# Performance work log

Measured on AMD Instinct MI355X. Metric: run time of the kernel, lower is better.

The kernel has to match this reference:

```python
import jax, jax.numpy as jnp
import numpy as np

WINDOW = 128
LOOK_BACKWARD = 1
LOOK_FORWARD = 0  # causal=True -> look_forward defaults to 0
THETA = 10000.0


def look_around(x, backward=LOOK_BACKWARD, forward=LOOK_FORWARD, pad_value=-1):
    # x: (b, w, n, ...). Pad along window axis, concat shifted slices along token axis.
    w = x.shape[1]
    pad_width = [(0, 0)] * x.ndim
    pad_width[1] = (backward, forward)
    padded = jnp.pad(x, pad_width, constant_values=pad_value)
    return jnp.concatenate([padded[:, i:i + w] for i in range(forward + backward + 1)], axis=2)


def rotate_half(x):
    x1, x2 = jnp.split(x, 2, axis=-1)
    return jnp.concatenate((-x2, x1), axis=-1)


def setup_inputs() -> dict:
    key = jax.random.key(0)
    kq, kk, kv = jax.random.split(key, 3)
    shape = (32, 4096, 64)
    return {
        "q": jax.random.normal(kq, shape, dtype=jnp.float32),
        "k": jax.random.normal(kk, shape, dtype=jnp.float32),
        "v": jax.random.normal(kv, shape, dtype=jnp.float32),
    }


def reference(q, k, v):
    b, n, d = q.shape
    scale = d ** -0.5
    w = n // WINDOW

    bq = q.reshape(b, w, WINDOW, d) * scale
    bk = look_around(k.reshape(b, w, WINDOW, d), pad_value=-1.0)
    bv = look_around(v.reshape(b, w, WINDOW, d), pad_value=-1.0)
    j = bk.shape[2]  # (1 + look_backward + look_forward) * WINDOW = 256

    # rotary pos emb (SinusoidalEmbeddings, no xpos -> scale = 1)
    inv_freq = 1.0 / (THETA ** (jnp.arange(0, d, 2, dtype=jnp.float32) / d))
    t = jnp.arange(j, dtype=jnp.float32)
    freqs = jnp.einsum('i,j->ij', t, inv_freq)
    freqs = jnp.concatenate((freqs, freqs), axis=-1)  # (j, d)
    q_freqs = freqs[-WINDOW:]  # queries align to the last WINDOW positions
    bq = bq * jnp.cos(q_freqs) + rotate_half(bq) * jnp.sin(q_freqs)
    bk = bk * jnp.cos(freqs) + rotate_half(bk) * jnp.sin(freqs)

    # position bookkeeping for masks
    seq = jnp.arange(n)
    b_t = seq.reshape(1, w, WINDOW)           # (1, w, i)
    bq_t = b_t[..., :, None]                  # (1, w, i, 1)
    bq_k = look_around(b_t, pad_value=-1)[..., None, :]  # (1, w, 1, j)
    pad_mask = bq_k == -1
    causal_mask = bq_t < bq_k

    sim = jnp.einsum('bwie,bwje->bwij', bq, bk)  # (b, w, i, j)
    mask_value = -jnp.finfo(sim.dtype).max
    sim = jnp.where(causal_mask | pad_mask, mask_value, sim)

    attn = jax.nn.softmax(sim, axis=-1)
    out = jnp.einsum('bwij,bwje->bwie', attn, bv)
    return out.reshape(b, n, d)
```

## Files before the change

kernel.cpp:

```cpp
#include <hip/hip_runtime.h>
#include <hip/hip_bf16.h>

#define BDIM 512

typedef __attribute__((ext_vector_type(8))) _Float16 f16x8;
typedef __attribute__((ext_vector_type(4))) _Float16 f16x4;
typedef __attribute__((ext_vector_type(4))) float f32x4;

__global__ __launch_bounds__(512, 4)
void la_kernel(const float* __restrict__ qg, const float* __restrict__ kg,
               const float* __restrict__ vg, float* __restrict__ outg)
{
    __shared__ _Float16 Ks[2][128][72];
    __shared__ _Float16 Vt[2][64][140];

    const int wp = blockIdx.x, bb = blockIdx.y;
    const int tid = threadIdx.x;
    const int wv = tid >> 6, lane = tid & 63, g = lane >> 4, c = lane & 15;
    const int base = 256 * wp - 128;
    const float NEG = -3.0e38f;
    const float NLT32 = -0.28782313662425572f;

    const int cbK = (tid & 7) << 2;
    float invfK[4];
    #pragma unroll
    for (int u = 0; u < 4; ++u) invfK[u] = __expf((float)(cbK + u) * NLT32);
    float invfQ[8];
    #pragma unroll
    for (int u = 0; u < 8; ++u) invfQ[u] = __expf((float)(8 * g + u) * NLT32);

    const int jqV = tid >> 4, eqV = tid & 15;
    const int colbV = ((jqV & 24) << 2) + 8 * (jqV & 3) + 4 * ((jqV >> 2) & 1);

    auto stage = [&](int mm) {
        int sl = mm & 1;
        #pragma unroll
        for (int it = 0; it < 2; ++it) {
            int j = (tid + it * 512) >> 3;
            int t = 128 * mm + j;
            const float* p = kg + ((size_t)bb * 4096 + base + t) * 64 + cbK;
            float4 x1 = *(const float4*)p;
            float4 x2 = *(const float4*)(p + 32);
            const float* x1p = &x1.x;
            const float* x2p = &x2.x;
            f16x4 lo, hi;
            #pragma unroll
            for (int u = 0; u < 4; ++u) {
                float sn, cs; __sincosf((float)t * invfK[u], &sn, &cs);
                lo[u] = (_Float16)(x1p[u] * cs - x2p[u] * sn);
                hi[u] = (_Float16)(x2p[u] * cs + x1p[u] * sn);
            }
            *(f16x4*)&Ks[sl][j][cbK]      = lo;
            *(f16x4*)&Ks[sl][j][cbK + 32] = hi;
        }
        float4 x[4];
        #pragma unroll
        for (int w = 0; w < 4; ++w)
            x[w] = *(const float4*)(vg + ((size_t)bb * 4096 + base + 128 * mm + 4 * jqV + w) * 64 + 4 * eqV);
        #pragma unroll
        for (int u = 0; u < 4; ++u) {
            f16x4 o;
            o[0] = (_Float16)((const float*)&x[0])[u];
            o[1] = (_Float16)((const float*)&x[1])[u];
            o[2] = (_Float16)((const float*)&x[2])[u];
            o[3] = (_Float16)((const float*)&x[3])[u];
            *(f16x4*)&Vt[sl][4 * eqV + u][colbV] = o;
        }
    };

    auto computeWin = [&](int wi) {
        const int qrow = tid < 0 ? 0 : (wv * 16 + c);
        const int tq = 128 * (wi + 1) + qrow;

        f16x8 qa0, qa1;
        {
            const float* p = qg + ((size_t)bb * 4096 + base + tq) * 64 + 8 * g;
            float4 a0 = *(const float4*)p;
            float4 a1 = *(const float4*)(p + 4);
            float4 b0 = *(const float4*)(p + 32);
            float4 b1 = *(const float4*)(p + 36);
            float ra[8] = {a0.x,a0.y,a0.z,a0.w,a1.x,a1.y,a1.z,a1.w};
            float rb[8] = {b0.x,b0.y,b0.z,b0.w,b1.x,b1.y,b1.z,b1.w};
            #pragma unroll
            for (int u = 0; u < 8; ++u) {
                float sn, cs; __sincosf((float)tq * invfQ[u], &sn, &cs);
                float a = ra[u] * 0.125f, b = rb[u] * 0.125f;
                qa0[u] = (_Float16)(a * cs - b * sn);
                qa1[u] = (_Float16)(b * cs + a * sn);
            }
        }

        f32x4 accO[4];
        #pragma unroll
        for (int nt = 0; nt < 4; ++nt) accO[nt] = (f32x4){0.f,0.f,0.f,0.f};
        float m = NEG, s = 0.f;

        #pragma unroll 1
        for (int mm = wi; mm <= wi + 1; ++mm) {
            if (wp == 0 && mm == 0) continue;
            const int sl = mm & 1;
            const bool causal = (mm == wi + 1);

            #pragma unroll
            for (int ch = 0; ch < 2; ++ch) {
                f32x4 acc[4];
                #pragma unroll
                for (int jt = 0; jt < 4; ++jt) acc[jt] = (f32x4){0.f,0.f,0.f,0.f};

                #pragma unroll
                for (int jt = 0; jt < 4; ++jt) {
                    int row = ch * 64 + jt * 16 + c;
                    f16x8 kb0 = *(const f16x8*)&Ks[sl][row][8 * g];
                    f16x8 kb1 = *(const f16x8*)&Ks[sl][row][32 + 8 * g];
                    acc[jt] = __builtin_amdgcn_mfma_f32_16x16x32_f16(kb0, qa0, acc[jt], 0, 0, 0);
                    acc[jt] = __builtin_amdgcn_mfma_f32_16x16x32_f16(kb1, qa1, acc[jt], 0, 0, 0);
                }

                if (causal) {
                    #pragma unroll
                    for (int jt = 0; jt < 4; ++jt)
                        #pragma unroll
                        for (int r = 0; r < 4; ++r) {
                            int jj = ch * 64 + jt * 16 + 4 * g + r;
                            if (jj > qrow) acc[jt][r] = NEG;
                        }
                }

                float mx = NEG;
                #pragma unroll
                for (int jt = 0; jt < 4; ++jt)
                    #pragma unroll
                    for (int r = 0; r < 4; ++r) mx = fmaxf(mx, acc[jt][r]);
                mx = fmaxf(mx, __shfl_xor(mx, 16));
                mx = fmaxf(mx, __shfl_xor(mx, 32));

                float mnew = fmaxf(m, mx);
                float alpha = __expf(m - mnew);

                float ps = 0.f;
                f16x8 pa[2];
                #pragma unroll
                for (int jt = 0; jt < 4; ++jt)
                    #pragma unroll
                    for (int r = 0; r < 4; ++r) {
                        float p = __expf(acc[jt][r] - mnew);
                        ps += p;
                        pa[jt >> 1][(jt & 1) * 4 + r] = (_Float16)p;
                    }
                ps += __shfl_xor(ps, 16);
                ps += __shfl_xor(ps, 32);

                s = s * alpha + ps;
                m = mnew;

                float alphaD[4];
                #pragma unroll
                for (int r = 0; r < 4; ++r)
                    alphaD[r] = __shfl(alpha, (lane & 48) | (4 * g + r));
                #pragma unroll
                for (int nt = 0; nt < 4; ++nt)
                    #pragma unroll
                    for (int r = 0; r < 4; ++r) accO[nt][r] *= alphaD[r];

                #pragma unroll
                for (int st = 0; st < 2; ++st) {
                    #pragma unroll
                    for (int nt = 0; nt < 4; ++nt) {
                        f16x8 vb = *(const f16x8*)&Vt[sl][nt * 16 + c][ch * 64 + st * 32 + 8 * g];
                        accO[nt] = __builtin_amdgcn_mfma_f32_16x16x32_f16(pa[st], vb, accO[nt], 0, 0, 0);
                    }
                }
            }
        }

        float rcp = 1.0f / s;
        float rcpD[4];
        #pragma unroll
        for (int r = 0; r < 4; ++r)
            rcpD[r] = __shfl(rcp, (lane & 48) | (4 * g + r));

        float* op = outg + ((size_t)bb * 4096 + base + 128 * (wi + 1) + wv * 16) * 64;
        #pragma unroll
        for (int nt = 0; nt < 4; ++nt)
            #pragma unroll
            for (int r = 0; r < 4; ++r)
                op[(size_t)(4 * g + r) * 64 + nt * 16 + c] = accO[nt][r] * rcpD[r];
    };

    if (wp > 0) stage(0);
    stage(1);
    __syncthreads();
    computeWin(0);
    __syncthreads();
    stage(2);
    __syncthreads();
    computeWin(1);
}

extern "C" void kernel_launch(void* const* d_in, const int* in_sizes, int n_in,
                              void* d_out, int out_size, void* d_ws, size_t ws_size,
                              hipStream_t stream) {
    (void)in_sizes; (void)n_in; (void)out_size; (void)d_ws; (void)ws_size;
    const float* q = (const float*)d_in[0];
    const float* k = (const float*)d_in[1];
    const float* v = (const float*)d_in[2];
    float* out = (float*)d_out;
    dim3 grid(16, 32);
    la_kernel<<<grid, BDIM, 0, stream>>>(q, k, v, out);
}
```

Before: 34.00 us.

## Prefetch third K/V chunk into registers during first window compute

The K and V global loads for the third chunk are now issued before the first window's compute, held in registers, and rotated and written to shared memory only after that compute finishes. The Q load for window 0 is hoisted before the barrier, and the Q load for window 1 is moved ahead of the final barrier. This is meant to hide global-memory latency behind the MFMA work instead of stalling between the two window computations. It adds about 32 registers per thread of live prefetch data, which could limit occupancy under launch_bounds(512,4).

```diff
diff --git a/kernel.cpp b/kernel.cpp
--- a/kernel.cpp
+++ b/kernel.cpp
@@ -20,6 +20,7 @@
     const int base = 256 * wp - 128;
     const float NEG = -3.0e38f;
     const float NLT32 = -0.28782313662425572f;
+    const size_t rowb = (size_t)bb * 4096;
 
     const int cbK = (tid & 7) << 2;
     float invfK[4];
@@ -32,13 +33,15 @@
     const int jqV = tid >> 4, eqV = tid & 15;
     const int colbV = ((jqV & 24) << 2) + 8 * (jqV & 3) + 4 * ((jqV >> 2) & 1);
 
+    const int qrow = wv * 16 + c;
+
     auto stage = [&](int mm) {
         int sl = mm & 1;
         #pragma unroll
         for (int it = 0; it < 2; ++it) {
             int j = (tid + it * 512) >> 3;
             int t = 128 * mm + j;
-            const float* p = kg + ((size_t)bb * 4096 + base + t) * 64 + cbK;
+            const float* p = kg + (rowb + base + t) * 64 + cbK;
             float4 x1 = *(const float4*)p;
             float4 x2 = *(const float4*)(p + 32);
             const float* x1p = &x1.x;
@@ -56,7 +59,7 @@
         float4 x[4];
         #pragma unroll
         for (int w = 0; w < 4; ++w)
-            x[w] = *(const float4*)(vg + ((size_t)bb * 4096 + base + 128 * mm + 4 * jqV + w) * 64 + 4 * eqV);
+            x[w] = *(const float4*)(vg + (rowb + base + 128 * mm + 4 * jqV + w) * 64 + 4 * eqV);
         #pragma unroll
         for (int u = 0; u < 4; ++u) {
             f16x4 o;
@@ -68,28 +71,25 @@
         }
     };
 
-    auto computeWin = [&](int wi) {
-        const int qrow = tid < 0 ? 0 : (wv * 16 + c);
+    auto loadQ = [&](int wi, f16x8& qa0, f16x8& qa1) {
         const int tq = 128 * (wi + 1) + qrow;
-
-        f16x8 qa0, qa1;
-        {
-            const float* p = qg + ((size_t)bb * 4096 + base + tq) * 64 + 8 * g;
-            float4 a0 = *(const float4*)p;
-            float4 a1 = *(const float4*)(p + 4);
-            float4 b0 = *(const float4*)(p + 32);
-            float4 b1 = *(const float4*)(p + 36);
-            float ra[8] = {a0.x,a0.y,a0.z,a0.w,a1.x,a1.y,a1.z,a1.w};
-            float rb[8] = {b0.x,b0.y,b0.z,b0.w,b1.x,b1.y,b1.z,b1.w};
-            #pragma unroll
-            for (int u = 0; u < 8; ++u) {
-                float sn, cs; __sincosf((float)tq * invfQ[u], &sn, &cs);
-                float a = ra[u] * 0.125f, b = rb[u] * 0.125f;
-                qa0[u] = (_Float16)(a * cs - b * sn);
-                qa1[u] = (_Float16)(b * cs + a * sn);
-            }
-        }
-
+        const float* p = qg + (rowb + base + tq) * 64 + 8 * g;
+        float4 a0 = *(const float4*)p;
+        float4 a1 = *(const float4*)(p + 4);
+        float4 b0 = *(const float4*)(p + 32);
+        float4 b1 = *(const float4*)(p + 36);
+        float ra[8] = {a0.x,a0.y,a0.z,a0.w,a1.x,a1.y,a1.z,a1.w};
+        float rb[8] = {b0.x,b0.y,b0.z,b0.w,b1.x,b1.y,b1.z,b1.w};
+        #pragma unroll
+        for (int u = 0; u < 8; ++u) {
+            float sn, cs; __sincosf((float)tq * invfQ[u], &sn, &cs);
+            float a = ra[u] * 0.125f, b = rb[u] * 0.125f;
+            qa0[u] = (_Float16)(a * cs - b * sn);
+            qa1[u] = (_Float16)(b * cs + a * sn);
+        }
+    };
+
+    auto computeWin = [&](int wi, f16x8 qa0, f16x8 qa1) {
         f32x4 accO[4];
         #pragma unroll
         for (int nt = 0; nt < 4; ++nt) accO[nt] = (f32x4){0.f,0.f,0.f,0.f};
@@ -179,7 +179,7 @@
         for (int r = 0; r < 4; ++r)
             rcpD[r] = __shfl(rcp, (lane & 48) | (4 * g + r));
 
-        float* op = outg + ((size_t)bb * 4096 + base + 128 * (wi + 1) + wv * 16) * 64;
+        float* op = outg + (rowb + base + 128 * (wi + 1) + wv * 16) * 64;
         #pragma unroll
         for (int nt = 0; nt < 4; ++nt)
             #pragma unroll
@@ -189,12 +189,60 @@
 
     if (wp > 0) stage(0);
     stage(1);
+
+    f16x8 qA, qB;
+    loadQ(0, qA, qB);
+
+    float4 kx[4], vx[4];
+    {
+        #pragma unroll
+        for (int it = 0; it < 2; ++it) {
+            int j = (tid + it * 512) >> 3;
+            const float* p = kg + (rowb + base + 256 + j) * 64 + cbK;
+            kx[2 * it]     = *(const float4*)p;
+            kx[2 * it + 1] = *(const float4*)(p + 32);
+        }
+        #pragma unroll
+        for (int w = 0; w < 4; ++w)
+            vx[w] = *(const float4*)(vg + (rowb + base + 256 + 4 * jqV + w) * 64 + 4 * eqV);
+    }
+
     __syncthreads();
-    computeWin(0);
+    computeWin(0, qA, qB);
     __syncthreads();
-    stage(2);
+
+    {
+        #pragma unroll
+        for (int it = 0; it < 2; ++it) {
+            int j = (tid + it * 512) >> 3;
+            int t = 256 + j;
+            const float* x1p = (const float*)&kx[2 * it];
+            const float* x2p = (const float*)&kx[2 * it + 1];
+            f16x4 lo, hi;
+            #pragma unroll
+            for (int u = 0; u < 4; ++u) {
+                float sn, cs; __sincosf((float)t * invfK[u], &sn, &cs);
+                lo[u] = (_Float16)(x1p[u] * cs - x2p[u] * sn);
+                hi[u] = (_Float16)(x2p[u] * cs + x1p[u] * sn);
+            }
+            *(f16x4*)&Ks[0][j][cbK]      = lo;
+            *(f16x4*)&Ks[0][j][cbK + 32] = hi;
+        }
+        #pragma unroll
+        for (int u = 0; u < 4; ++u) {
+            f16x4 o;
+            o[0] = (_Float16)((const float*)&vx[0])[u];
+            o[1] = (_Float16)((const float*)&vx[1])[u];
+            o[2] = (_Float16)((const float*)&vx[2])[u];
+            o[3] = (_Float16)((const float*)&vx[3])[u];
+            *(f16x4*)&Vt[0][4 * eqV + u][colbV] = o;
+        }
+    }
+
+    loadQ(1, qA, qB);
+
     __syncthreads();
-    computeWin(1);
+    computeWin(1, qA, qB);
 }
 
 extern "C" void kernel_launch(void* const* d_in, const int* in_sizes, int n_in,
```

Measured after the change: 36.38 us. 1.07x slower.

## Skip fully masked causal chunks, use exp2 softmax, prefetch Q earlier

Applied to the files above, without the earlier changes.

Waves whose query rows all sit below the second 64-key chunk of the diagonal window now skip that chunk's QK and PV MFMAs entirely. The softmax switches to exp2 by folding log2(e) into the Q scale. It also skips the rescale of the output accumulator when no row's running max grows, tested wave-wide with __all. Q loads are issued before K/V staging and the barriers so global latency overlaps other work. The cost is extra branching plus slightly different rounding from the base-2 exponent path.

```diff
diff --git a/kernel.cpp b/kernel.cpp
--- a/kernel.cpp
+++ b/kernel.cpp
@@ -6,6 +6,8 @@
 typedef __attribute__((ext_vector_type(8))) _Float16 f16x8;
 typedef __attribute__((ext_vector_type(4))) _Float16 f16x4;
 typedef __attribute__((ext_vector_type(4))) float f32x4;
+
+#define EXP2F(x) __builtin_amdgcn_exp2f(x)
 
 __global__ __launch_bounds__(512, 4)
 void la_kernel(const float* __restrict__ qg, const float* __restrict__ kg,
@@ -20,6 +22,8 @@
     const int base = 256 * wp - 128;
     const float NEG = -3.0e38f;
     const float NLT32 = -0.28782313662425572f;
+    const float QSCALE = 0.125f * 1.4426950408889634f;
+    const size_t rowb = (size_t)bb * 4096;
 
     const int cbK = (tid & 7) << 2;
     float invfK[4];
@@ -32,13 +36,15 @@
     const int jqV = tid >> 4, eqV = tid & 15;
     const int colbV = ((jqV & 24) << 2) + 8 * (jqV & 3) + 4 * ((jqV >> 2) & 1);
 
+    const int qrow = wv * 16 + c;
+
     auto stage = [&](int mm) {
         int sl = mm & 1;
         #pragma unroll
         for (int it = 0; it < 2; ++it) {
             int j = (tid + it * 512) >> 3;
             int t = 128 * mm + j;
-            const float* p = kg + ((size_t)bb * 4096 + base + t) * 64 + cbK;
+            const float* p = kg + (rowb + base + t) * 64 + cbK;
             float4 x1 = *(const float4*)p;
             float4 x2 = *(const float4*)(p + 32);
             const float* x1p = &x1.x;
@@ -56,7 +62,7 @@
         float4 x[4];
         #pragma unroll
         for (int w = 0; w < 4; ++w)
-            x[w] = *(const float4*)(vg + ((size_t)bb * 4096 + base + 128 * mm + 4 * jqV + w) * 64 + 4 * eqV);
+            x[w] = *(const float4*)(vg + (rowb + base + 128 * mm + 4 * jqV + w) * 64 + 4 * eqV);
         #pragma unroll
         for (int u = 0; u < 4; ++u) {
             f16x4 o;
@@ -68,28 +74,28 @@
         }
     };
 
-    auto computeWin = [&](int wi) {
-        const int qrow = tid < 0 ? 0 : (wv * 16 + c);
+    auto loadQraw = [&](int wi, float4* qr) {
         const int tq = 128 * (wi + 1) + qrow;
-
-        f16x8 qa0, qa1;
-        {
-            const float* p = qg + ((size_t)bb * 4096 + base + tq) * 64 + 8 * g;
-            float4 a0 = *(const float4*)p;
-            float4 a1 = *(const float4*)(p + 4);
-            float4 b0 = *(const float4*)(p + 32);
-            float4 b1 = *(const float4*)(p + 36);
-            float ra[8] = {a0.x,a0.y,a0.z,a0.w,a1.x,a1.y,a1.z,a1.w};
-            float rb[8] = {b0.x,b0.y,b0.z,b0.w,b1.x,b1.y,b1.z,b1.w};
-            #pragma unroll
-            for (int u = 0; u < 8; ++u) {
-                float sn, cs; __sincosf((float)tq * invfQ[u], &sn, &cs);
-                float a = ra[u] * 0.125f, b = rb[u] * 0.125f;
-                qa0[u] = (_Float16)(a * cs - b * sn);
-                qa1[u] = (_Float16)(b * cs + a * sn);
-            }
-        }
-
+        const float* p = qg + (rowb + base + tq) * 64 + 8 * g;
+        qr[0] = *(const float4*)p;
+        qr[1] = *(const float4*)(p + 4);
+        qr[2] = *(const float4*)(p + 32);
+        qr[3] = *(const float4*)(p + 36);
+    };
+    auto ropeQ = [&](int wi, const float4* qr, f16x8& qa0, f16x8& qa1) {
+        const int tq = 128 * (wi + 1) + qrow;
+        float ra[8] = {qr[0].x,qr[0].y,qr[0].z,qr[0].w,qr[1].x,qr[1].y,qr[1].z,qr[1].w};
+        float rb[8] = {qr[2].x,qr[2].y,qr[2].z,qr[2].w,qr[3].x,qr[3].y,qr[3].z,qr[3].w};
+        #pragma unroll
+        for (int u = 0; u < 8; ++u) {
+            float sn, cs; __sincosf((float)tq * invfQ[u], &sn, &cs);
+            float a = ra[u] * QSCALE, b = rb[u] * QSCALE;
+            qa0[u] = (_Float16)(a * cs - b * sn);
+            qa1[u] = (_Float16)(b * cs + a * sn);
+        }
+    };
+
+    auto computeWin = [&](int wi, f16x8 qa0, f16x8 qa1) {
         f32x4 accO[4];
         #pragma unroll
         for (int nt = 0; nt < 4; ++nt) accO[nt] = (f32x4){0.f,0.f,0.f,0.f};
@@ -103,6 +109,8 @@
 
             #pragma unroll
             for (int ch = 0; ch < 2; ++ch) {
+                if (causal && ch == 1 && wv < 4) continue;
+
                 f32x4 acc[4];
                 #pragma unroll
                 for (int jt = 0; jt < 4; ++jt) acc[jt] = (f32x4){0.f,0.f,0.f,0.f};
@@ -134,8 +142,8 @@
                 mx = fmaxf(mx, __shfl_xor(mx, 16));
                 mx = fmaxf(mx, __shfl_xor(mx, 32));
 
-                float mnew = fmaxf(m, mx);
-                float alpha = __expf(m - mnew);
+                const bool grow = !__all(mx <= m);
+                float mnew = grow ? fmaxf(m, mx) : m;
 
                 float ps = 0.f;
                 f16x8 pa[2];
@@ -143,24 +151,28 @@
                 for (int jt = 0; jt < 4; ++jt)
                     #pragma unroll
                     for (int r = 0; r < 4; ++r) {
-                        float p = __expf(acc[jt][r] - mnew);
+                        float p = EXP2F(acc[jt][r] - mnew);
                         ps += p;
                         pa[jt >> 1][(jt & 1) * 4 + r] = (_Float16)p;
                     }
                 ps += __shfl_xor(ps, 16);
                 ps += __shfl_xor(ps, 32);
 
-                s = s * alpha + ps;
-                m = mnew;
-
-                float alphaD[4];
-                #pragma unroll
-                for (int r = 0; r < 4; ++r)
-                    alphaD[r] = __shfl(alpha, (lane & 48) | (4 * g + r));
-                #pragma unroll
-                for (int nt = 0; nt < 4; ++nt)
-                    #pragma unroll
-                    for (int r = 0; r < 4; ++r) accO[nt][r] *= alphaD[r];
+                if (grow) {
+                    float alpha = EXP2F(m - mnew);
+                    s = s * alpha + ps;
+                    m = mnew;
+                    float alphaD[4];
+                    #pragma unroll
+                    for (int r = 0; r < 4; ++r)
+                        alphaD[r] = __shfl(alpha, (lane & 48) | (4 * g + r));
+                    #pragma unroll
+                    for (int nt = 0; nt < 4; ++nt)
+                        #pragma unroll
+                        for (int r = 0; r < 4; ++r) accO[nt][r] *= alphaD[r];
+                } else {
+                    s += ps;
+                }
 
                 #pragma unroll
                 for (int st = 0; st < 2; ++st) {
@@ -179,7 +191,7 @@
         for (int r = 0; r < 4; ++r)
             rcpD[r] = __shfl(rcp, (lane & 48) | (4 * g + r));
 
-        float* op = outg + ((size_t)bb * 4096 + base + 128 * (wi + 1) + wv * 16) * 64;
+        float* op = outg + (rowb + base + 128 * (wi + 1) + wv * 16) * 64;
         #pragma unroll
         for (int nt = 0; nt < 4; ++nt)
             #pragma unroll
@@ -187,14 +199,20 @@
                 op[(size_t)(4 * g + r) * 64 + nt * 16 + c] = accO[nt][r] * rcpD[r];
     };
 
+    float4 qr[4];
+    loadQraw(0, qr);
     if (wp > 0) stage(0);
     stage(1);
+    f16x8 qA, qB;
+    ropeQ(0, qr, qA, qB);
     __syncthreads();
-    computeWin(0);
+    computeWin(0, qA, qB);
+    loadQraw(1, qr);
     __syncthreads();
     stage(2);
+    ropeQ(1, qr, qA, qB);
     __syncthreads();
-    computeWin(1);
+    computeWin(1, qA, qB);
 }
 
 extern "C" void kernel_launch(void* const* d_in, const int* in_sizes, int n_in,
```

Result: faster. 33.24 us (-2.2%).
